# Performance work log

Hardware: AMD Instinct MI355X
Metric: run time of the kernel (lower is better)

## Reference

```python
import jax, jax.numpy as jnp
import numpy as np

EPS = 1e-5

def _ste(x, q):
    # straight-through estimator: forward=q, backward=identity
    return x + jax.lax.stop_gradient(q - x)

def act_quant(x):
    # per-token int8 absmax quantization (BitNet b1.58 style), fake-quantized
    scale = 127.0 / jnp.clip(jnp.max(jnp.abs(x), axis=-1, keepdims=True), EPS)
    q = jnp.clip(jnp.round(x * scale), -128.0, 127.0) / scale
    return _ste(x, q)

def weight_quant(w):
    # ternary {-1,0,1} weights scaled by mean absolute value
    s = jnp.clip(jnp.mean(jnp.abs(w)), EPS)
    q = jnp.clip(jnp.round(w / s), -1.0, 1.0) * s
    return _ste(w, q)

def bit_linear(x, w):
    # x: [..., in], w: [out, in]
    return jnp.einsum('bsi,oi->bso', act_quant(x), weight_quant(w))

def setup_inputs() -> dict:
    key = jax.random.key(0)
    k1, k2, k3 = jax.random.split(key, 3)
    d_model, hidden = 2048, 4 * 2048
    x = jax.random.normal(k1, (4, 2048, d_model), dtype=jnp.float32)
    w1 = jax.random.normal(k2, (hidden, d_model), dtype=jnp.float32) * 0.02
    w2 = jax.random.normal(k3, (d_model, hidden), dtype=jnp.float32) * 0.02
    return {"x": x, "w1": w1, "w2": w2}

def reference(x, w1, w2):
    h = bit_linear(x, w1)            # [B, S, 4*d]
    h = jax.nn.gelu(h, approximate=False)  # exact erf GELU (nn.GELU default)
    return bit_linear(h, w2)         # [B, S, d]
```

## Files before the change

kernel.cpp:

```cpp
#include <hip/hip_runtime.h>
#include <hip/hip_bf16.h>
#include <hip/hip_fp16.h>
#include <stdint.h>

#define TPB 256
#define EPSF 1e-5f

using i32x4 = __attribute__((ext_vector_type(4))) int;


__device__ __forceinline__ void gload16(const void* g, void* l) {
    __builtin_amdgcn_global_load_lds(
        (__attribute__((address_space(1))) void*)g,
        (__attribute__((address_space(3))) void*)l,
        16, 0, 0);
}

__device__ __forceinline__ float wave_reduce_sum(float v) {
#pragma unroll
    for (int off = 32; off > 0; off >>= 1) v += __shfl_down(v, off, 64);
    return v;
}

__device__ __forceinline__ float wave_reduce_max(float v) {
#pragma unroll
    for (int off = 32; off > 0; off >>= 1) v = fmaxf(v, __shfl_down(v, off, 64));
    return v;
}

__device__ __forceinline__ int q8(float f, float scale, float lo, float hi) {
    return (int)fminf(fmaxf(rintf(f * scale), lo), hi);
}

__device__ __forceinline__ float gelu_fast(float x) {
    float x2 = x * x;
    float u = x * (0.7978845608f + 0.0356774081f * x2);
    float e = exp2f(u * -2.8853900817779268f);
    return x * __builtin_amdgcn_rcpf(1.0f + e);
}


__global__ void abssum2(const float* __restrict__ w1, const float* __restrict__ w2,
                        int n4, float* __restrict__ part) {
    const bool second = blockIdx.x >= 2048;
    const float4* w4 = (const float4*)(second ? w2 : w1);
    const int b = blockIdx.x & 2047;
    float acc = 0.f;
    for (int i = b * TPB + threadIdx.x; i < n4; i += 2048 * TPB) {
        float4 v = w4[i];
        acc += fabsf(v.x) + fabsf(v.y) + fabsf(v.z) + fabsf(v.w);
    }
    acc = wave_reduce_sum(acc);
    __shared__ float sh[4];
    if ((threadIdx.x & 63) == 0) sh[threadIdx.x >> 6] = acc;
    __syncthreads();
    if (threadIdx.x == 0) part[blockIdx.x] = sh[0] + sh[1] + sh[2] + sh[3];
}

__global__ void finalize_scales(const float* __restrict__ part,
                                float* __restrict__ scales, float inv_n) {
    float a = 0.f, b = 0.f;
    for (int i = threadIdx.x; i < 2048; i += TPB) { a += part[i]; b += part[i + 2048]; }
    a = wave_reduce_sum(a);
    b = wave_reduce_sum(b);
    __shared__ float sa[4], sb[4];
    if ((threadIdx.x & 63) == 0) { sa[threadIdx.x >> 6] = a; sb[threadIdx.x >> 6] = b; }
    __syncthreads();
    if (threadIdx.x == 0) {
        scales[0] = fmaxf((sa[0] + sa[1] + sa[2] + sa[3]) * inv_n, EPSF);
        scales[1] = fmaxf((sb[0] + sb[1] + sb[2] + sb[3]) * inv_n, EPSF);
    }
}


__global__ void quant_w_i8(const float* __restrict__ w,
                           signed char* __restrict__ wq,
                           const float* __restrict__ scales, int sidx, int n4) {
    const float inv = 1.0f / scales[sidx];
    const float4* w4 = (const float4*)w;
    unsigned* oq = (unsigned*)wq;
    for (int i = blockIdx.x * TPB + threadIdx.x; i < n4; i += gridDim.x * TPB) {
        float4 v = w4[i];
        unsigned p = ((unsigned)(q8(v.x, inv, -1.f, 1.f) & 0xff)) |
                     ((unsigned)(q8(v.y, inv, -1.f, 1.f) & 0xff) << 8) |
                     ((unsigned)(q8(v.z, inv, -1.f, 1.f) & 0xff) << 16) |
                     ((unsigned)(q8(v.w, inv, -1.f, 1.f) & 0xff) << 24);
        oq[i] = p;
    }
}


template <int NF4>
__global__ void quant_x_i8(const float* __restrict__ in,
                           signed char* __restrict__ outq,
                           float* __restrict__ dq, int cols) {
    const long long row = blockIdx.x;
    const float4* r4 = (const float4*)(in + row * (long long)cols);
    float4 v[NF4];
    float mx = 0.f;
#pragma unroll
    for (int j = 0; j < NF4; ++j) {
        v[j] = r4[threadIdx.x + TPB * j];
        mx = fmaxf(mx, fmaxf(fmaxf(fabsf(v[j].x), fabsf(v[j].y)),
                             fmaxf(fabsf(v[j].z), fabsf(v[j].w))));
    }
    mx = wave_reduce_max(mx);
    __shared__ float sh[4];
    __shared__ float res;
    if ((threadIdx.x & 63) == 0) sh[threadIdx.x >> 6] = mx;
    __syncthreads();
    if (threadIdx.x == 0) res = fmaxf(fmaxf(sh[0], sh[1]), fmaxf(sh[2], sh[3]));
    __syncthreads();
    const float clipped = fmaxf(res, EPSF);
    const float scale = 127.f / clipped;
    if (threadIdx.x == 0) dq[row] = clipped / 127.f;
    unsigned* oq = (unsigned*)(outq + row * (long long)cols);
#pragma unroll
    for (int j = 0; j < NF4; ++j) {
        unsigned p = ((unsigned)(q8(v[j].x, scale, -128.f, 127.f) & 0xff)) |
                     ((unsigned)(q8(v[j].y, scale, -128.f, 127.f) & 0xff) << 8) |
                     ((unsigned)(q8(v[j].z, scale, -128.f, 127.f) & 0xff) << 16) |
                     ((unsigned)(q8(v[j].w, scale, -128.f, 127.f) & 0xff) << 24);
        oq[threadIdx.x + TPB * j] = p;
    }
}


template <int NJ>
__global__ void quant_h_i8(const unsigned short* __restrict__ h,
                           signed char* __restrict__ outq,
                           float* __restrict__ dq, int cols) {
    const long long row = blockIdx.x;
    const unsigned short* rp = h + row * (long long)cols;
    uint4 v[NJ];
    float mx = 0.f;
#pragma unroll
    for (int j = 0; j < NJ; ++j) {
        v[j] = *(const uint4*)(rp + (threadIdx.x + TPB * j) * 8);
        const unsigned* u = (const unsigned*)&v[j];
#pragma unroll
        for (int e = 0; e < 4; ++e) {
            float2 f2 = __half22float2(*(const __half2*)&u[e]);
            mx = fmaxf(mx, fmaxf(fabsf(f2.x), fabsf(f2.y)));
        }
    }
    mx = wave_reduce_max(mx);
    __shared__ float sh[4];
    __shared__ float res;
    if ((threadIdx.x & 63) == 0) sh[threadIdx.x >> 6] = mx;
    __syncthreads();
    if (threadIdx.x == 0) res = fmaxf(fmaxf(sh[0], sh[1]), fmaxf(sh[2], sh[3]));
    __syncthreads();
    const float clipped = fmaxf(res, EPSF);
    const float scale = 127.f / clipped;
    if (threadIdx.x == 0) dq[row] = clipped / 127.f;
    uint2* oq = (uint2*)(outq + row * (long long)cols);
#pragma unroll
    for (int j = 0; j < NJ; ++j) {
        const unsigned* u = (const unsigned*)&v[j];
        unsigned o[2] = {0, 0};
#pragma unroll
        for (int e = 0; e < 4; ++e) {
            float2 f2 = __half22float2(*(const __half2*)&u[e]);
            unsigned b0 = (unsigned)(q8(f2.x, scale, -128.f, 127.f) & 0xff);
            unsigned b1 = (unsigned)(q8(f2.y, scale, -128.f, 127.f) & 0xff);
            o[e >> 1] |= (b0 | (b1 << 8)) << ((e & 1) * 16);
        }
        oq[threadIdx.x + TPB * j] = *(uint2*)o;
    }
}


__device__ __forceinline__ void stage_half(const char* Xb, long long rowB, int prow,
                                           int tk, char* dst, int tid, int cbs) {
    const long long gc = (long long)tk * 128 + cbs;
    const int r = tid >> 3;
    gload16(Xb + (long long)(prow + r) * rowB + gc, dst + tid * 16);
    gload16(Xb + (long long)(prow + 64 + r) * rowB + gc, dst + 8192 + tid * 16);
}

#define QUAD(MB, NB)                                                            \
    _Pragma("unroll") for (int mi = 0; mi < 4; ++mi)                            \
    _Pragma("unroll") for (int ni = 0; ni < 2; ++ni)                            \
    _Pragma("unroll") for (int ks = 0; ks < 2; ++ks)                            \
        acc[(MB)*4 + mi][(NB)*2 + ni] = __builtin_amdgcn_mfma_i32_16x16x64_i8(  \
            aq[mi][ks], bq[(NB)*2 + ni][ks], acc[(MB)*4 + mi][(NB)*2 + ni], 0, 0, 0);

#define READ_A(base_mi)                                                         \
    _Pragma("unroll") for (int mi = 0; mi < 4; ++mi) {                          \
        const char* p = cur + aoff + ((mi + (base_mi)) * 16 + l15) * 128;       \
        aq[mi][0] = *(const i32x4*)(p + acb0);                                  \
        aq[mi][1] = *(const i32x4*)(p + acb1);                                  \
    }
#define READ_B(n0i, n1i)                                                        \
    _Pragma("unroll") for (int ni = (n0i); ni < (n1i); ++ni) {                  \
        const char* p = cur + boff + (ni * 16 + l15) * 128;                     \
        bq[ni][0] = *(const i32x4*)(p + acb0);                                  \
        bq[ni][1] = *(const i32x4*)(p + acb1);                                  \
    }


__global__ __launch_bounds__(512, 2) void gemm1p(
    const signed char* __restrict__ A, const signed char* __restrict__ B,
    unsigned short* __restrict__ C, int N, int K,
    const float* __restrict__ dq, const float* __restrict__ scales, int ntile) {
    __shared__ __align__(16) char lds[131072];

    const int tid = threadIdx.x;
    const int lane = tid & 63;
    const int wid = tid >> 6;
    const int wr = wid >> 2;
    const int wc = wid & 3;

    const unsigned orig = blockIdx.y * gridDim.x + blockIdx.x;
    const unsigned xk = orig & 7, j = orig >> 3;
    const unsigned bx = (xk & 3) * 8 + (j & 7);
    const unsigned byg = (xk >> 2) * 4 + (j >> 3);

    const int n0 = (int)bx * 256;
    const long long rb = (long long)K;
    const char* Ab = (const char*)A;
    const char* Bb = (const char*)B;

    const int NTT = ntile << 4;

    const int cbs = (((tid & 7) ^ ((tid >> 3) & 7)) << 4);
    const int l15 = lane & 15, l4 = lane >> 4;
    const int swz = (lane & 7) << 4;
    const int acb0 = (l4 * 16) ^ swz;
    const int acb1 = (64 + l4 * 16) ^ swz;
    const int aoff = wr * 16384;
    const int boff = 32768 + (wc >> 1) * 16384 + (wc & 1) * 8192;

    i32x4 acc[8][4] = {};
    i32x4 aq[4][2], bq[4][2];

    auto mrow = [&](int v) -> int { return ((int)byg * ntile + (v >> 4)) * 256; };

    stage_half(Bb, rb, n0, 0, lds + 32768, tid, cbs);
    stage_half(Bb, rb, n0 + 128, 0, lds + 32768 + 16384, tid, cbs);
    stage_half(Ab, rb, mrow(0), 0, lds + 0, tid, cbs);
    stage_half(Ab, rb, mrow(0) + 128, 0, lds + 16384, tid, cbs);
    stage_half(Bb, rb, n0, 1, lds + 65536 + 32768, tid, cbs);
    stage_half(Bb, rb, n0 + 128, 1, lds + 65536 + 32768 + 16384, tid, cbs);
    stage_half(Ab, rb, mrow(1), 1, lds + 65536, tid, cbs);
    asm volatile("s_waitcnt vmcnt(6)" ::: "memory");
    __builtin_amdgcn_sched_barrier(0);
    __builtin_amdgcn_s_barrier();

    const float s = scales[0];

    for (int vt = 0; vt < NTT; ++vt) {
        char* cur = lds + ((vt & 1) << 16);
        char* nxt = lds + (((vt + 1) & 1) << 16);
        const bool s1 = (vt + 1) < NTT;
        const bool s2 = (vt + 2) < NTT;
        const int k1 = (vt + 1) & 15;
        const int k2 = (vt + 2) & 15;

        READ_A(0);
        READ_B(0, 2);
        if (s1) stage_half(Ab, rb, mrow(vt + 1) + 128, k1, nxt + 16384, tid, cbs);
        __builtin_amdgcn_s_setprio(1);
        QUAD(0, 0);
        __builtin_amdgcn_s_setprio(0);
        __builtin_amdgcn_s_barrier();

        READ_B(2, 4);
        if (s2) stage_half(Bb, rb, n0, k2, cur + 32768, tid, cbs);
        __builtin_amdgcn_s_setprio(1);
        QUAD(0, 1);
        __builtin_amdgcn_s_setprio(0);
        __builtin_amdgcn_s_barrier();

        READ_A(4);
        if (s2) stage_half(Bb, rb, n0 + 128, k2, cur + 32768 + 16384, tid, cbs);
        __builtin_amdgcn_s_setprio(1);
        QUAD(1, 0);
        __builtin_amdgcn_s_setprio(0);
        __builtin_amdgcn_s_barrier();

        if (s2) stage_half(Ab, rb, mrow(vt + 2), k2, cur, tid, cbs);
        __builtin_amdgcn_s_setprio(1);
        QUAD(1, 1);
        __builtin_amdgcn_s_setprio(0);
        if (s2) { asm volatile("s_waitcnt vmcnt(6)" ::: "memory"); }
        else    { asm volatile("s_waitcnt vmcnt(0)" ::: "memory"); }
        __builtin_amdgcn_sched_barrier(0);
        __builtin_amdgcn_s_barrier();

        if ((vt & 15) == 15) {
            const int m0 = mrow(vt);
#pragma unroll
            for (int mi = 0; mi < 8; ++mi) {
#pragma unroll
                for (int r = 0; r < 4; ++r) {
                    const long long m = m0 + wr * 128 + mi * 16 + l4 * 4 + r;
                    const float f = dq[m] * s;
#pragma unroll
                    for (int ni = 0; ni < 4; ++ni) {
                        const long long n = n0 + wc * 64 + ni * 16 + l15;
                        float v = gelu_fast((float)acc[mi][ni][r] * f);
                        __half hh = __float2half(v);
                        C[m * (long long)N + n] = *(const unsigned short*)&hh;
                        acc[mi][ni][r] = 0;
                    }
                }
            }
        }
    }
}


__global__ __launch_bounds__(512, 2) void gemm2k(
    const signed char* __restrict__ A, const signed char* __restrict__ B,
    float* __restrict__ C, int N, int K,
    const float* __restrict__ dq, const float* __restrict__ scales) {
    __shared__ __align__(16) char lds[131072];

    const int tid = threadIdx.x;
    const int lane = tid & 63;
    const int wid = tid >> 6;
    const int wr = wid >> 2;
    const int wc = wid & 3;

    const unsigned gx = gridDim.x;
    unsigned lin = blockIdx.y * gx + blockIdx.x;
    const unsigned qq = (gx * gridDim.y) >> 3;
    lin = (lin & 7) * qq + (lin >> 3);
    const unsigned bx = lin % gx;
    const unsigned by = lin / gx;

    const long long M0 = (long long)by * 256;
    const long long N0 = (long long)bx * 256;
    const long long rb = (long long)K;
    const char* Ab = (const char*)A + M0 * rb;
    const char* Bb = (const char*)B + N0 * rb;
    const int nt = K >> 7;

    const int cbs = (((tid & 7) ^ ((tid >> 3) & 7)) << 4);
    const int l15 = lane & 15, l4 = lane >> 4;
    const int swz = (lane & 7) << 4;
    const int acb0 = (l4 * 16) ^ swz;
    const int acb1 = (64 + l4 * 16) ^ swz;
    const int aoff = wr * 16384;
    const int boff = 32768 + (wc >> 1) * 16384 + (wc & 1) * 8192;

    i32x4 acc[8][4] = {};
    i32x4 aq[4][2], bq[4][2];

    stage_half(Bb, rb, 0,   0, lds + 32768,         tid, cbs);
    stage_half(Bb, rb, 128, 0, lds + 32768 + 16384, tid, cbs);
    stage_half(Ab, rb, 0,   0, lds + 0,             tid, cbs);
    stage_half(Ab, rb, 128, 0, lds + 16384,         tid, cbs);
    stage_half(Bb, rb, 0,   1, lds + 65536 + 32768,         tid, cbs);
    stage_half(Bb, rb, 128, 1, lds + 65536 + 32768 + 16384, tid, cbs);
    stage_half(Ab, rb, 0,   1, lds + 65536,                 tid, cbs);
    asm volatile("s_waitcnt vmcnt(6)" ::: "memory");
    __builtin_amdgcn_sched_barrier(0);
    __builtin_amdgcn_s_barrier();

    for (int t = 0; t < nt; ++t) {
        char* cur = lds + ((t & 1) << 16);
        char* nxt = lds + (((t + 1) & 1) << 16);
        const bool s1 = (t + 1) < nt;
        const bool s2 = (t + 2) < nt;

        READ_A(0);
        READ_B(0, 2);
        if (s1) stage_half(Ab, rb, 128, t + 1, nxt + 16384, tid, cbs);
        __builtin_amdgcn_s_setprio(1);
        QUAD(0, 0);
        __builtin_amdgcn_s_setprio(0);
        __builtin_amdgcn_s_barrier();

        READ_B(2, 4);
        if (s2) stage_half(Bb, rb, 0, t + 2, cur + 32768, tid, cbs);
        __builtin_amdgcn_s_setprio(1);
        QUAD(0, 1);
        __builtin_amdgcn_s_setprio(0);
        __builtin_amdgcn_s_barrier();

        READ_A(4);
        if (s2) stage_half(Bb, rb, 128, t + 2, cur + 32768 + 16384, tid, cbs);
        __builtin_amdgcn_s_setprio(1);
        QUAD(1, 0);
        __builtin_amdgcn_s_setprio(0);
        __builtin_amdgcn_s_barrier();

        if (s2) stage_half(Ab, rb, 0, t + 2, cur, tid, cbs);
        __builtin_amdgcn_s_setprio(1);
        QUAD(1, 1);
        __builtin_amdgcn_s_setprio(0);
        if (s2) { asm volatile("s_waitcnt vmcnt(6)" ::: "memory"); }
        else    { asm volatile("s_waitcnt vmcnt(0)" ::: "memory"); }
        __builtin_amdgcn_sched_barrier(0);
        __builtin_amdgcn_s_barrier();
    }

    const float s = scales[1];
#pragma unroll
    for (int mi = 0; mi < 8; ++mi) {
#pragma unroll
        for (int r = 0; r < 4; ++r) {
            const long long m = M0 + wr * 128 + mi * 16 + l4 * 4 + r;
            const float f = dq[m] * s;
#pragma unroll
            for (int ni = 0; ni < 4; ++ni) {
                const long long n = N0 + wc * 64 + ni * 16 + l15;
                __builtin_nontemporal_store(
                    (float)acc[mi][ni][r] * f, C + m * (long long)N + n);
            }
        }
    }
}


extern "C" void kernel_launch(void* const* d_in, const int* in_sizes, int n_in,
                              void* d_out, int out_size, void* d_ws, size_t ws_size,
                              hipStream_t stream) {
    (void)n_in; (void)out_size;
    const float* x  = (const float*)d_in[0];
    const float* w1 = (const float*)d_in[1];
    const float* w2 = (const float*)d_in[2];
    float* out = (float*)d_out;

    const int D = 2048, H = 8192;
    const long long M = (long long)in_sizes[0] / D;

    char* base = (char*)d_ws;
    size_t off = 0;
    auto alloc = [&](size_t bytes) -> char* {
        char* r = base + off;
        off = (off + bytes + 255) & ~(size_t)255;
        return r;
    };

    const bool fullM = ws_size >= (size_t)236 * 1024 * 1024;
    const long long MC = fullM ? M : M / 2;

    float* part = (float*)alloc(4096 * 4);
    float* scales = (float*)alloc(256);
    float* dqx = (float*)alloc((size_t)M * 4);
    float* dqh = (float*)alloc((size_t)M * 4);
    signed char* wq = (signed char*)alloc((size_t)H * D);
    signed char* xq = (signed char*)alloc((size_t)M * D);
    signed char* hq = (signed char*)alloc((size_t)M * H);
    unsigned short* hf = (unsigned short*)alloc((size_t)MC * H * 2);

    const int nw4 = H * D / 4;
    abssum2<<<4096, TPB, 0, stream>>>(w1, w2, nw4, part);
    finalize_scales<<<1, TPB, 0, stream>>>(part, scales, 1.0f / (float)(H * D));
    quant_w_i8<<<2048, TPB, 0, stream>>>(w1, wq, scales, 0, nw4);
    quant_x_i8<2><<<(int)M, TPB, 0, stream>>>(x, xq, dqx, D);

    if (fullM) {
        gemm1p<<<dim3(32, 8), 512, 0, stream>>>(xq, wq, hf, H, D, dqx, scales, 4);
        quant_h_i8<4><<<(int)M, TPB, 0, stream>>>(hf, hq, dqh, H);
    } else {
        for (int g = 0; g < 2; ++g) {
            const long long m0 = g * MC;
            gemm1p<<<dim3(32, 8), 512, 0, stream>>>(
                xq + m0 * D, wq, hf, H, D, dqx + m0, scales, 2);
            quant_h_i8<4><<<(int)MC, TPB, 0, stream>>>(hf, hq + m0 * H, dqh + m0, H);
        }
    }

    quant_w_i8<<<2048, TPB, 0, stream>>>(w2, wq, scales, 1, nw4);

    gemm2k<<<dim3(D / 256, (int)(M / 256)), 512, 0, stream>>>(
        hq, wq, out, D, H, dqh, scales);
}
```

Before: 358.1 us.

## Split GEMM epilogues into halves overlapped with remaining MFMA work

Each GEMM's epilogue is split into two halves. The top half of the accumulator rows (mi 0-3) is written during the last k-step, once those accumulators are final and before QUAD(1,0) runs. The bottom half (mi 4-7) is emitted during the first step of the next persistent tile, or after the loop. This interleaves the GELU and global stores with MFMA work instead of running them serially at tile boundaries. In exchange, the schedule is more complex, and emitting inside the barrier-synchronised phases may stretch phase times or raise register pressure.

```diff
diff --git a/kernel.cpp b/kernel.cpp
--- a/kernel.cpp
+++ b/kernel.cpp
@@ -199,6 +199,21 @@
         bq[ni][1] = *(const i32x4*)(p + acb1);                                  \
     }
 
+#define EMIT1(MLO, MHI, M0V)                                                    \
+    _Pragma("unroll") for (int mi = (MLO); mi < (MHI); ++mi) {                  \
+        _Pragma("unroll") for (int r = 0; r < 4; ++r) {                         \
+            const long long m = (M0V) + wr * 128 + mi * 16 + l4 * 4 + r;        \
+            const float f = dq[m] * s;                                          \
+            _Pragma("unroll") for (int ni = 0; ni < 4; ++ni) {                  \
+                const long long n = n0 + wc * 64 + ni * 16 + l15;               \
+                float v = gelu_fast((float)acc[mi][ni][r] * f);                 \
+                __half hh = __float2half(v);                                    \
+                C[m * (long long)N + n] = *(const unsigned short*)&hh;          \
+                acc[mi][ni][r] = 0;                                             \
+            }                                                                   \
+        }                                                                       \
+    }
+
 
 __global__ __launch_bounds__(512, 2) void gemm1p(
     const signed char* __restrict__ A, const signed char* __restrict__ B,
@@ -255,12 +270,14 @@
         char* nxt = lds + (((vt + 1) & 1) << 16);
         const bool s1 = (vt + 1) < NTT;
         const bool s2 = (vt + 2) < NTT;
+        const int kk = vt & 15;
         const int k1 = (vt + 1) & 15;
         const int k2 = (vt + 2) & 15;
 
         READ_A(0);
         READ_B(0, 2);
         if (s1) stage_half(Ab, rb, mrow(vt + 1) + 128, k1, nxt + 16384, tid, cbs);
+        if (kk == 0 && vt > 0) { EMIT1(4, 8, mrow(vt - 1)); }
         __builtin_amdgcn_s_setprio(1);
         QUAD(0, 0);
         __builtin_amdgcn_s_setprio(0);
@@ -275,6 +292,7 @@
 
         READ_A(4);
         if (s2) stage_half(Bb, rb, n0 + 128, k2, cur + 32768 + 16384, tid, cbs);
+        if (kk == 15) { EMIT1(0, 4, mrow(vt)); }
         __builtin_amdgcn_s_setprio(1);
         QUAD(1, 0);
         __builtin_amdgcn_s_setprio(0);
@@ -288,29 +306,24 @@
         else    { asm volatile("s_waitcnt vmcnt(0)" ::: "memory"); }
         __builtin_amdgcn_sched_barrier(0);
         __builtin_amdgcn_s_barrier();
-
-        if ((vt & 15) == 15) {
-            const int m0 = mrow(vt);
-#pragma unroll
-            for (int mi = 0; mi < 8; ++mi) {
-#pragma unroll
-                for (int r = 0; r < 4; ++r) {
-                    const long long m = m0 + wr * 128 + mi * 16 + l4 * 4 + r;
-                    const float f = dq[m] * s;
-#pragma unroll
-                    for (int ni = 0; ni < 4; ++ni) {
-                        const long long n = n0 + wc * 64 + ni * 16 + l15;
-                        float v = gelu_fast((float)acc[mi][ni][r] * f);
-                        __half hh = __float2half(v);
-                        C[m * (long long)N + n] = *(const unsigned short*)&hh;
-                        acc[mi][ni][r] = 0;
-                    }
-                }
-            }
-        }
-    }
-}
-
+    }
+
+    { EMIT1(4, 8, mrow(NTT - 1)); }
+}
+
+
+#define EMIT2(MLO, MHI)                                                         \
+    _Pragma("unroll") for (int mi = (MLO); mi < (MHI); ++mi) {                  \
+        _Pragma("unroll") for (int r = 0; r < 4; ++r) {                         \
+            const long long m = M0 + wr * 128 + mi * 16 + l4 * 4 + r;           \
+            const float f = dq[m] * s;                                          \
+            _Pragma("unroll") for (int ni = 0; ni < 4; ++ni) {                  \
+                const long long n = N0 + wc * 64 + ni * 16 + l15;               \
+                __builtin_nontemporal_store(                                    \
+                    (float)acc[mi][ni][r] * f, C + m * (long long)N + n);       \
+            }                                                                   \
+        }                                                                       \
+    }
 
 __global__ __launch_bounds__(512, 2) void gemm2k(
     const signed char* __restrict__ A, const signed char* __restrict__ B,
@@ -360,6 +373,8 @@
     __builtin_amdgcn_sched_barrier(0);
     __builtin_amdgcn_s_barrier();
 
+    const float s = scales[1];
+
     for (int t = 0; t < nt; ++t) {
         char* cur = lds + ((t & 1) << 16);
         char* nxt = lds + (((t + 1) & 1) << 16);
@@ -383,6 +398,7 @@
 
         READ_A(4);
         if (s2) stage_half(Bb, rb, 128, t + 2, cur + 32768 + 16384, tid, cbs);
+        if (t == nt - 1) { EMIT2(0, 4); }
         __builtin_amdgcn_s_setprio(1);
         QUAD(1, 0);
         __builtin_amdgcn_s_setprio(0);
@@ -398,21 +414,7 @@
         __builtin_amdgcn_s_barrier();
     }
 
-    const float s = scales[1];
-#pragma unroll
-    for (int mi = 0; mi < 8; ++mi) {
-#pragma unroll
-        for (int r = 0; r < 4; ++r) {
-            const long long m = M0 + wr * 128 + mi * 16 + l4 * 4 + r;
-            const float f = dq[m] * s;
-#pragma unroll
-            for (int ni = 0; ni < 4; ++ni) {
-                const long long n = N0 + wc * 64 + ni * 16 + l15;
-                __builtin_nontemporal_store(
-                    (float)acc[mi][ni][r] * f, C + m * (long long)N + n);
-            }
-        }
-    }
+    { EMIT2(4, 8); }
 }
 
 
```

New measurement: 357.6 us. About the same (-0.1%).
